# Optimization experiments

Hardware: AMD Instinct MI355X
Metric: run time of the kernel (lower is better)

The kernel has to match this reference:

```python
import jax, jax.numpy as jnp
import numpy as np

B, S, D_IN, H, D_HEAD = 4, 1024, 768, 12, 64


def setup_inputs() -> dict:
    key = jax.random.key(0)
    k1, k2, k3, k4 = jax.random.split(key, 4)
    x = jax.random.normal(k1, (B, S, D_IN), dtype=jnp.float32)
    # Per-head projection weights stored as [H, d_in, d_head] (equivalent to
    # nn.Linear weight [d_head, d_in] applied as x @ W.T), scaled like default init.
    scale = 1.0 / np.sqrt(D_IN)
    Wq = jax.random.normal(k2, (H, D_IN, D_HEAD), dtype=jnp.float32) * scale
    Wk = jax.random.normal(k3, (H, D_IN, D_HEAD), dtype=jnp.float32) * scale
    Wv = jax.random.normal(k4, (H, D_IN, D_HEAD), dtype=jnp.float32) * scale
    return {"x": x, "Wq": Wq, "Wk": Wk, "Wv": Wv}


def reference(x, Wq, Wk, Wv):
    # Vectorized over heads; faithful to per-head causal attention then concat.
    q = jnp.einsum("bsd,hde->bhse", x, Wq)  # [B,H,S,Dh]
    k = jnp.einsum("bsd,hde->bhse", x, Wk)
    v = jnp.einsum("bsd,hde->bhse", x, Wv)
    scale = 1.0 / jnp.sqrt(jnp.asarray(D_HEAD, dtype=q.dtype))
    scores = jnp.einsum("bhse,bhte->bhst", q, k) * scale  # [B,H,S,S]
    causal = jnp.tril(jnp.ones((S, S), dtype=bool))
    scores = jnp.where(causal, scores, jnp.finfo(scores.dtype).min)
    attn = jax.nn.softmax(scores, axis=-1)  # dropout p=0.0 (eval) -> identity
    ctx = jnp.einsum("bhst,bhte->bhse", attn, v)  # [B,H,S,Dh]
    # concat heads along last dim: [B,S,H*Dh]
    return jnp.transpose(ctx, (0, 2, 1, 3)).reshape(B, S, H * D_HEAD)
```

## Files before the change

kernel.cpp:

```cpp
#include <hip/hip_runtime.h>
#include <hip/hip_bf16.h>

#define NB 4
#define SS 1024
#define DIN 768
#define NH 12
#define DH 64

typedef float f32x4 __attribute__((ext_vector_type(4)));
typedef short bf16x8 __attribute__((ext_vector_type(8)));

static __device__ __forceinline__ unsigned short f2bf(float f) {
    __hip_bfloat16 h = __float2bfloat16(f);
    return *reinterpret_cast<unsigned short*>(&h);
}

static __device__ __forceinline__ float exp2_fast(float x) {
    return __builtin_amdgcn_exp2f(x);
}

static __device__ __forceinline__ void gload16(const void* g, void* l) {
    __builtin_amdgcn_global_load_lds(
        (const __attribute__((address_space(1))) void*)g,
        (__attribute__((address_space(3))) void*)l, 16, 0, 0);
}

__global__ void cast_x_kernel(const float* __restrict__ x, unsigned short* __restrict__ xb) {
    int i = (blockIdx.x * 256 + threadIdx.x) * 4;
    float4 v = *reinterpret_cast<const float4*>(x + i);
    ushort4 o;
    o.x = f2bf(v.x); o.y = f2bf(v.y); o.z = f2bf(v.z); o.w = f2bf(v.w);
    *reinterpret_cast<ushort4*>(xb + i) = o;
}

__global__ void transpose_w_kernel(const float* __restrict__ Wq, const float* __restrict__ Wk,
                                   const float* __restrict__ Wv, unsigned short* __restrict__ wt) {
    __shared__ float lds[64][68];
    int d0 = blockIdx.x * 64;
    int h  = blockIdx.y;
    int p  = blockIdx.z;
    const float* W = (p == 0) ? Wq : (p == 1) ? Wk : Wv;
    const float* base = W + (size_t)h * DIN * DH;
    int tid = threadIdx.x;
    int rr = tid >> 4, c4 = tid & 15;
#pragma unroll
    for (int i = 0; i < 4; ++i) {
        int d = i * 16 + rr;
        float4 v = *reinterpret_cast<const float4*>(base + (size_t)(d0 + d) * DH + c4 * 4);
        lds[d][c4 * 4 + 0] = v.x; lds[d][c4 * 4 + 1] = v.y;
        lds[d][c4 * 4 + 2] = v.z; lds[d][c4 * 4 + 3] = v.w;
    }
    __syncthreads();
    unsigned short* outp = wt + ((size_t)(p * NH + h) * DH) * DIN;
#pragma unroll
    for (int i = 0; i < 4; ++i) {
        int e = i * 16 + rr;
        int dc = c4 * 4;
        ushort4 o;
        o.x = f2bf(lds[dc + 0][e]); o.y = f2bf(lds[dc + 1][e]);
        o.z = f2bf(lds[dc + 2][e]); o.w = f2bf(lds[dc + 3][e]);
        *reinterpret_cast<ushort4*>(outp + (size_t)e * DIN + d0 + dc) = o;
    }
}

__global__ __launch_bounds__(256) void qkv_gemm_kernel(
    const unsigned short* __restrict__ xb, const unsigned short* __restrict__ wt,
    unsigned short* __restrict__ qb, unsigned short* __restrict__ kb,
    unsigned short* __restrict__ vT) {
    __shared__ __align__(16) unsigned char smem[28672];
    unsigned short* a_lds = (unsigned short*)smem;
    unsigned short* b_lds = (unsigned short*)(smem + 16384);

    int m0 = blockIdx.x * 128;
    int n0 = blockIdx.y * 96;
    int tid = threadIdx.x, lane = tid & 63, w = tid >> 6;
    int l15 = lane & 15, hi4 = (lane >> 4) * 4, hi8 = (lane >> 4) * 8;
    int wr = w >> 1, wc = w & 1;
    int srow = tid >> 3;
    int scolb = (tid & 7) * 16;
    int sw = (l15 & 7) << 4;

    f32x4 acc[4][3] = {};

    for (int k0 = 0; k0 < DIN; k0 += 64) {
        __syncthreads();
#pragma unroll
        for (int i = 0; i < 4; ++i) {
            int row = i * 32 + srow;
            int cb = scolb ^ ((row & 7) << 4);
            gload16(xb + (size_t)(m0 + row) * DIN + k0 + (cb >> 1), a_lds + row * 64 + (scolb >> 1));
        }
#pragma unroll
        for (int i = 0; i < 3; ++i) {
            int row = i * 32 + srow;
            int cb = scolb ^ ((row & 7) << 4);
            gload16(wt + (size_t)(n0 + row) * DIN + k0 + (cb >> 1), b_lds + row * 64 + (scolb >> 1));
        }
        __syncthreads();
#pragma unroll
        for (int kk = 0; kk < 64; kk += 32) {
            int cb = ((kk + hi8) * 2) ^ sw;
            bf16x8 af[4], bfr[3];
#pragma unroll
            for (int m = 0; m < 4; ++m)
                af[m] = *reinterpret_cast<const bf16x8*>(a_lds + (wr * 64 + m * 16 + l15) * 64 + (cb >> 1));
#pragma unroll
            for (int n = 0; n < 3; ++n)
                bfr[n] = *reinterpret_cast<const bf16x8*>(b_lds + (wc * 48 + n * 16 + l15) * 64 + (cb >> 1));
#pragma unroll
            for (int m = 0; m < 4; ++m)
#pragma unroll
                for (int n = 0; n < 3; ++n)
                    acc[m][n] = __builtin_amdgcn_mfma_f32_16x16x32_bf16(af[m], bfr[n], acc[m][n], 0, 0, 0);
        }
    }
    __syncthreads();

    int p  = n0 / 768;
    int cp = (n0 % 768) + wc * 48;
    int b  = m0 >> 10;
    int s_base = (m0 & 1023) + wr * 64;

    if (p < 2) {
        float qs = (p == 0) ? 0.180336880f : 1.0f;
        unsigned short* dstb = (p == 0) ? qb : kb;
#pragma unroll
        for (int m = 0; m < 4; ++m)
#pragma unroll
            for (int n = 0; n < 3; ++n)
#pragma unroll
                for (int r = 0; r < 4; ++r) {
                    int col = cp + n * 16 + l15;
                    int h = col >> 6, e = col & 63;
                    dstb[((size_t)(b * NH + h) * SS + s_base + m * 16 + hi4 + r) * DH + e] =
                        f2bf(acc[m][n][r] * qs);
                }
    } else {
        float* sc = (float*)smem + w * 784;
#pragma unroll
        for (int m = 0; m < 4; ++m) {
#pragma unroll
            for (int n = 0; n < 3; ++n)
#pragma unroll
                for (int r = 0; r < 4; ++r)
                    sc[(hi4 + r) * 49 + n * 16 + l15] = acc[m][n][r];
            if (lane < 48) {
                unsigned short vv[16];
#pragma unroll
                for (int t = 0; t < 16; ++t) vv[t] = f2bf(sc[t * 49 + lane]);
                int col = cp + lane;
                int h = col >> 6, e = col & 63;
                unsigned short* dst = vT + ((size_t)(b * NH + h) * DH + e) * SS + s_base + m * 16;
                *reinterpret_cast<uint4*>(dst)     = *reinterpret_cast<const uint4*>(vv);
                *reinterpret_cast<uint4*>(dst + 8) = *reinterpret_cast<const uint4*>(vv + 8);
            }
        }
    }
}

struct AttnCtx {
    const unsigned short* kg;
    const unsigned short* vg;
    unsigned short* k0lds; unsigned short* k1lds;
    unsigned short* v0lds; unsigned short* v1lds;
    unsigned short* pw;
    int srow, scolb, l15, hi4, hi8, sw;
};

static __device__ __forceinline__ void attn_stage(const AttnCtx& c, int buf, int kv) {
    unsigned short* kl = buf ? c.k1lds : c.k0lds;
    unsigned short* vl = buf ? c.v1lds : c.v0lds;
#pragma unroll
    for (int i = 0; i < 2; ++i) {
        int row = i * 32 + c.srow;
        int cb = c.scolb ^ ((row & 7) << 4);
        gload16(c.kg + (size_t)(kv * 64 + row) * DH + (cb >> 1), kl + row * 64 + (c.scolb >> 1));
        gload16(c.vg + (size_t)row * SS + kv * 64 + (cb >> 1),   vl + row * 64 + (c.scolb >> 1));
    }
}

template<bool DIAG>
static __device__ __forceinline__ void attn_step(
    const AttnCtx& c, int buf, int kv, int row_q,
    bf16x8 qf0, bf16x8 qf1, float m_r[4], float l_r[4], f32x4 o_acc[4]) {
    const unsigned short* kl = buf ? c.k1lds : c.k0lds;
    const unsigned short* vl = buf ? c.v1lds : c.v0lds;
    int l15 = c.l15, hi4 = c.hi4, hi8 = c.hi8, sw = c.sw;

    f32x4 sacc[4] = {};
#pragma unroll
    for (int s = 0; s < 2; ++s) {
        int cb = ((32 * s + hi8) * 2) ^ sw;
#pragma unroll
        for (int n = 0; n < 4; ++n) {
            bf16x8 kf = *reinterpret_cast<const bf16x8*>(kl + (16 * n + l15) * 64 + (cb >> 1));
            sacc[n] = __builtin_amdgcn_mfma_f32_16x16x32_bf16(s == 0 ? qf0 : qf1, kf, sacc[n], 0, 0, 0);
        }
    }
    float pv[4][4];
#pragma unroll
    for (int n = 0; n < 4; ++n)
#pragma unroll
        for (int r = 0; r < 4; ++r) {
            float sv = sacc[n][r];
            if (DIAG && (kv * 64 + 16 * n + l15) > (row_q + hi4 + r)) sv = -INFINITY;
            pv[n][r] = sv;
        }
#pragma unroll
    for (int r = 0; r < 4; ++r) {
        float mx = fmaxf(fmaxf(pv[0][r], pv[1][r]), fmaxf(pv[2][r], pv[3][r]));
        mx = fmaxf(mx, __shfl_xor(mx, 1));
        mx = fmaxf(mx, __shfl_xor(mx, 2));
        mx = fmaxf(mx, __shfl_xor(mx, 4));
        mx = fmaxf(mx, __shfl_xor(mx, 8));
        float m_new = fmaxf(m_r[r], mx);
        float s0 = exp2_fast(pv[0][r] - m_new);
        float s1 = exp2_fast(pv[1][r] - m_new);
        float s2 = exp2_fast(pv[2][r] - m_new);
        float s3 = exp2_fast(pv[3][r] - m_new);
        pv[0][r] = s0; pv[1][r] = s1; pv[2][r] = s2; pv[3][r] = s3;
        float sum = (s0 + s1) + (s2 + s3);
        sum += __shfl_xor(sum, 1);
        sum += __shfl_xor(sum, 2);
        sum += __shfl_xor(sum, 4);
        sum += __shfl_xor(sum, 8);
        float alpha = exp2_fast(m_r[r] - m_new);
        l_r[r] = l_r[r] * alpha + sum;
        m_r[r] = m_new;
#pragma unroll
        for (int n = 0; n < 4; ++n) o_acc[n][r] *= alpha;
    }
#pragma unroll
    for (int n = 0; n < 4; ++n)
#pragma unroll
        for (int r = 0; r < 4; ++r)
            c.pw[(hi4 + r) * 72 + 16 * n + l15] = f2bf(pv[n][r]);
    bf16x8 pa0 = *reinterpret_cast<const bf16x8*>(c.pw + l15 * 72 + hi8);
    bf16x8 pa1 = *reinterpret_cast<const bf16x8*>(c.pw + l15 * 72 + 32 + hi8);
#pragma unroll
    for (int s = 0; s < 2; ++s) {
        int cb = ((32 * s + hi8) * 2) ^ sw;
#pragma unroll
        for (int n = 0; n < 4; ++n) {
            bf16x8 vf = *reinterpret_cast<const bf16x8*>(vl + (16 * n + l15) * 64 + (cb >> 1));
            o_acc[n] = __builtin_amdgcn_mfma_f32_16x16x32_bf16(s == 0 ? pa0 : pa1, vf, o_acc[n], 0, 0, 0);
        }
    }
}

__global__ __launch_bounds__(256) void attn_kernel(
    const unsigned short* __restrict__ qb, const unsigned short* __restrict__ kb,
    const unsigned short* __restrict__ vT, float* __restrict__ out) {
    __shared__ __align__(16) unsigned short k_lds[2][64 * 64];
    __shared__ __align__(16) unsigned short v_lds[2][64 * 64];
    __shared__ __align__(16) unsigned short p_lds[4 * 16 * 72];

    int bid = blockIdx.x;
    int qi = 15 - bid / 48;
    int rem = bid % 48;
    int h = rem % 12, b = rem / 12;
    int q0 = qi * 64;
    int tid = threadIdx.x, lane = tid & 63, w = tid >> 6;
    int l15 = lane & 15, hi4 = (lane >> 4) * 4, hi8 = (lane >> 4) * 8;
    size_t bh = (size_t)(b * NH + h);

    AttnCtx c;
    c.kg = kb + bh * SS * DH;
    c.vg = vT + bh * DH * SS;
    c.k0lds = k_lds[0]; c.k1lds = k_lds[1];
    c.v0lds = v_lds[0]; c.v1lds = v_lds[1];
    c.pw = p_lds + w * 16 * 72;
    c.srow = tid >> 3; c.scolb = (tid & 7) * 16;
    c.l15 = l15; c.hi4 = hi4; c.hi8 = hi8; c.sw = (l15 & 7) << 4;

    const unsigned short* qp = qb + (bh * SS + q0 + 16 * w + l15) * DH;
    bf16x8 qf0 = *reinterpret_cast<const bf16x8*>(qp + hi8);
    bf16x8 qf1 = *reinterpret_cast<const bf16x8*>(qp + 32 + hi8);

    float m_r[4] = {-INFINITY, -INFINITY, -INFINITY, -INFINITY};
    float l_r[4] = {0.f, 0.f, 0.f, 0.f};
    f32x4 o_acc[4] = {};
    int row_q = q0 + 16 * w;

    attn_stage(c, 0, 0);
    __syncthreads();
    for (int kv = 0; kv < qi; ++kv) {
        int cur = kv & 1;
        attn_stage(c, cur ^ 1, kv + 1);
        attn_step<false>(c, cur, kv, row_q, qf0, qf1, m_r, l_r, o_acc);
        __syncthreads();
    }
    attn_step<true>(c, qi & 1, qi, row_q, qf0, qf1, m_r, l_r, o_acc);

    float inv[4];
#pragma unroll
    for (int r = 0; r < 4; ++r) inv[r] = 1.f / l_r[r];
#pragma unroll
    for (int n = 0; n < 4; ++n)
#pragma unroll
        for (int r = 0; r < 4; ++r) {
            int q = q0 + 16 * w + hi4 + r;
            int e = 16 * n + l15;
            out[((size_t)b * SS + q) * (NH * DH) + h * DH + e] = o_acc[n][r] * inv[r];
        }
}

extern "C" void kernel_launch(void* const* d_in, const int* in_sizes, int n_in,
                              void* d_out, int out_size, void* d_ws, size_t ws_size,
                              hipStream_t stream) {
    const float* x  = (const float*)d_in[0];
    const float* Wq = (const float*)d_in[1];
    const float* Wk = (const float*)d_in[2];
    const float* Wv = (const float*)d_in[3];
    float* out = (float*)d_out;

    char* ws = (char*)d_ws;
    unsigned short* xb = (unsigned short*)ws;
    unsigned short* wt = (unsigned short*)(ws +  6291456);
    unsigned short* qb = (unsigned short*)(ws +  9830400);
    unsigned short* kb = (unsigned short*)(ws + 16121856);
    unsigned short* vT = (unsigned short*)(ws + 22413312);

    hipLaunchKernelGGL(cast_x_kernel,      dim3(3072),      dim3(256), 0, stream, x, xb);
    hipLaunchKernelGGL(transpose_w_kernel, dim3(12, 12, 3), dim3(256), 0, stream, Wq, Wk, Wv, wt);
    hipLaunchKernelGGL(qkv_gemm_kernel,    dim3(32, 24),    dim3(256), 0, stream, xb, wt, qb, kb, vT);
    hipLaunchKernelGGL(attn_kernel,        dim3(768),       dim3(256), 0, stream, qb, kb, vT, out);
}
```

Measured before the change: 124.8 us.

## Transpose attention MFMA operands, lazy softmax rescale, vectorized output store

Swaps the MFMA operand order so each lane owns one query row. The softmax max and sum reductions now need only two cross-lane shuffles, and each lane holds a single m/l scalar instead of four. The running-max rescale is skipped unless some row's max grows by more than 8 (log2 units), which cuts exp and multiply work but lets the unnormalized values grow up to 2^8. It also adds s_setprio around the MFMA blocks and packs P writes as 32-bit words. The output goes through an LDS transpose so it can be written with 16-byte vector stores.

```diff
diff --git a/kernel.cpp b/kernel.cpp
--- a/kernel.cpp
+++ b/kernel.cpp
@@ -161,15 +161,14 @@
 struct AttnCtx {
     const unsigned short* kg;
     const unsigned short* vg;
-    unsigned short* k0lds; unsigned short* k1lds;
-    unsigned short* v0lds; unsigned short* v1lds;
+    char* smem;
     unsigned short* pw;
-    int srow, scolb, l15, hi4, hi8, sw;
+    int srow, scolb, l15, hi, sw;
 };
 
 static __device__ __forceinline__ void attn_stage(const AttnCtx& c, int buf, int kv) {
-    unsigned short* kl = buf ? c.k1lds : c.k0lds;
-    unsigned short* vl = buf ? c.v1lds : c.v0lds;
+    unsigned short* kl = (unsigned short*)(c.smem + buf * 8192);
+    unsigned short* vl = (unsigned short*)(c.smem + 16384 + buf * 8192);
 #pragma unroll
     for (int i = 0; i < 2; ++i) {
         int row = i * 32 + c.srow;
@@ -181,79 +180,95 @@
 
 template<bool DIAG>
 static __device__ __forceinline__ void attn_step(
-    const AttnCtx& c, int buf, int kv, int row_q,
-    bf16x8 qf0, bf16x8 qf1, float m_r[4], float l_r[4], f32x4 o_acc[4]) {
-    const unsigned short* kl = buf ? c.k1lds : c.k0lds;
-    const unsigned short* vl = buf ? c.v1lds : c.v0lds;
-    int l15 = c.l15, hi4 = c.hi4, hi8 = c.hi8, sw = c.sw;
+    const AttnCtx& c, int buf, int kv, int qg,
+    bf16x8 qf0, bf16x8 qf1, float& m_r, float& l_r, f32x4 o_acc[4]) {
+    const unsigned short* kl = (const unsigned short*)(c.smem + buf * 8192);
+    const unsigned short* vl = (const unsigned short*)(c.smem + 16384 + buf * 8192);
+    int l15 = c.l15, hi = c.hi, sw = c.sw;
+    int hi4 = hi * 4, hi8 = hi * 8;
 
     f32x4 sacc[4] = {};
+    __builtin_amdgcn_s_setprio(1);
 #pragma unroll
     for (int s = 0; s < 2; ++s) {
         int cb = ((32 * s + hi8) * 2) ^ sw;
 #pragma unroll
         for (int n = 0; n < 4; ++n) {
             bf16x8 kf = *reinterpret_cast<const bf16x8*>(kl + (16 * n + l15) * 64 + (cb >> 1));
-            sacc[n] = __builtin_amdgcn_mfma_f32_16x16x32_bf16(s == 0 ? qf0 : qf1, kf, sacc[n], 0, 0, 0);
-        }
-    }
+            sacc[n] = __builtin_amdgcn_mfma_f32_16x16x32_bf16(kf, s == 0 ? qf0 : qf1, sacc[n], 0, 0, 0);
+        }
+    }
+    __builtin_amdgcn_s_setprio(0);
+
     float pv[4][4];
 #pragma unroll
     for (int n = 0; n < 4; ++n)
 #pragma unroll
         for (int r = 0; r < 4; ++r) {
             float sv = sacc[n][r];
-            if (DIAG && (kv * 64 + 16 * n + l15) > (row_q + hi4 + r)) sv = -INFINITY;
+            if (DIAG && (kv * 64 + 16 * n + hi4 + r) > qg) sv = -INFINITY;
             pv[n][r] = sv;
         }
-#pragma unroll
-    for (int r = 0; r < 4; ++r) {
-        float mx = fmaxf(fmaxf(pv[0][r], pv[1][r]), fmaxf(pv[2][r], pv[3][r]));
-        mx = fmaxf(mx, __shfl_xor(mx, 1));
-        mx = fmaxf(mx, __shfl_xor(mx, 2));
-        mx = fmaxf(mx, __shfl_xor(mx, 4));
-        mx = fmaxf(mx, __shfl_xor(mx, 8));
-        float m_new = fmaxf(m_r[r], mx);
-        float s0 = exp2_fast(pv[0][r] - m_new);
-        float s1 = exp2_fast(pv[1][r] - m_new);
-        float s2 = exp2_fast(pv[2][r] - m_new);
-        float s3 = exp2_fast(pv[3][r] - m_new);
-        pv[0][r] = s0; pv[1][r] = s1; pv[2][r] = s2; pv[3][r] = s3;
-        float sum = (s0 + s1) + (s2 + s3);
-        sum += __shfl_xor(sum, 1);
-        sum += __shfl_xor(sum, 2);
-        sum += __shfl_xor(sum, 4);
-        sum += __shfl_xor(sum, 8);
-        float alpha = exp2_fast(m_r[r] - m_new);
-        l_r[r] = l_r[r] * alpha + sum;
-        m_r[r] = m_new;
-#pragma unroll
-        for (int n = 0; n < 4; ++n) o_acc[n][r] *= alpha;
-    }
+
+    float mn[4];
 #pragma unroll
     for (int n = 0; n < 4; ++n)
-#pragma unroll
-        for (int r = 0; r < 4; ++r)
-            c.pw[(hi4 + r) * 72 + 16 * n + l15] = f2bf(pv[n][r]);
+        mn[n] = fmaxf(fmaxf(pv[n][0], pv[n][1]), fmaxf(pv[n][2], pv[n][3]));
+    float mx = fmaxf(fmaxf(mn[0], mn[1]), fmaxf(mn[2], mn[3]));
+    mx = fmaxf(mx, __shfl_xor(mx, 16));
+    mx = fmaxf(mx, __shfl_xor(mx, 32));
+
+    if (!__all(mx - m_r <= 8.0f)) {
+        float m_new = fmaxf(m_r, mx);
+        float alpha = exp2_fast(m_r - m_new);
+        l_r *= alpha;
+#pragma unroll
+        for (int n = 0; n < 4; ++n)
+#pragma unroll
+            for (int r = 0; r < 4; ++r) o_acc[n][r] *= alpha;
+        m_r = m_new;
+    }
+    float sn[4];
+#pragma unroll
+    for (int n = 0; n < 4; ++n) {
+#pragma unroll
+        for (int r = 0; r < 4; ++r) pv[n][r] = exp2_fast(pv[n][r] - m_r);
+        sn[n] = (pv[n][0] + pv[n][1]) + (pv[n][2] + pv[n][3]);
+    }
+    float sum = (sn[0] + sn[1]) + (sn[2] + sn[3]);
+    sum += __shfl_xor(sum, 16);
+    sum += __shfl_xor(sum, 32);
+    l_r += sum;
+
+    unsigned int* pwu = (unsigned int*)c.pw;
+#pragma unroll
+    for (int n = 0; n < 4; ++n)
+#pragma unroll
+        for (int p2 = 0; p2 < 2; ++p2) {
+            unsigned int w32 = (unsigned int)f2bf(pv[n][2 * p2]) |
+                               ((unsigned int)f2bf(pv[n][2 * p2 + 1]) << 16);
+            pwu[l15 * 36 + 8 * n + 2 * hi + p2] = w32;
+        }
     bf16x8 pa0 = *reinterpret_cast<const bf16x8*>(c.pw + l15 * 72 + hi8);
     bf16x8 pa1 = *reinterpret_cast<const bf16x8*>(c.pw + l15 * 72 + 32 + hi8);
+
+    __builtin_amdgcn_s_setprio(1);
 #pragma unroll
     for (int s = 0; s < 2; ++s) {
         int cb = ((32 * s + hi8) * 2) ^ sw;
 #pragma unroll
         for (int n = 0; n < 4; ++n) {
             bf16x8 vf = *reinterpret_cast<const bf16x8*>(vl + (16 * n + l15) * 64 + (cb >> 1));
-            o_acc[n] = __builtin_amdgcn_mfma_f32_16x16x32_bf16(s == 0 ? pa0 : pa1, vf, o_acc[n], 0, 0, 0);
-        }
-    }
+            o_acc[n] = __builtin_amdgcn_mfma_f32_16x16x32_bf16(vf, s == 0 ? pa0 : pa1, o_acc[n], 0, 0, 0);
+        }
+    }
+    __builtin_amdgcn_s_setprio(0);
 }
 
 __global__ __launch_bounds__(256) void attn_kernel(
     const unsigned short* __restrict__ qb, const unsigned short* __restrict__ kb,
     const unsigned short* __restrict__ vT, float* __restrict__ out) {
-    __shared__ __align__(16) unsigned short k_lds[2][64 * 64];
-    __shared__ __align__(16) unsigned short v_lds[2][64 * 64];
-    __shared__ __align__(16) unsigned short p_lds[4 * 16 * 72];
+    __shared__ __align__(16) char smem[41984];
 
     int bid = blockIdx.x;
     int qi = 15 - bid / 48;
@@ -261,48 +276,49 @@
     int h = rem % 12, b = rem / 12;
     int q0 = qi * 64;
     int tid = threadIdx.x, lane = tid & 63, w = tid >> 6;
-    int l15 = lane & 15, hi4 = (lane >> 4) * 4, hi8 = (lane >> 4) * 8;
+    int l15 = lane & 15, hi = lane >> 4;
     size_t bh = (size_t)(b * NH + h);
 
     AttnCtx c;
     c.kg = kb + bh * SS * DH;
     c.vg = vT + bh * DH * SS;
-    c.k0lds = k_lds[0]; c.k1lds = k_lds[1];
-    c.v0lds = v_lds[0]; c.v1lds = v_lds[1];
-    c.pw = p_lds + w * 16 * 72;
+    c.smem = smem;
+    c.pw = (unsigned short*)(smem + 32768) + w * 1152;
     c.srow = tid >> 3; c.scolb = (tid & 7) * 16;
-    c.l15 = l15; c.hi4 = hi4; c.hi8 = hi8; c.sw = (l15 & 7) << 4;
-
-    const unsigned short* qp = qb + (bh * SS + q0 + 16 * w + l15) * DH;
-    bf16x8 qf0 = *reinterpret_cast<const bf16x8*>(qp + hi8);
-    bf16x8 qf1 = *reinterpret_cast<const bf16x8*>(qp + 32 + hi8);
-
-    float m_r[4] = {-INFINITY, -INFINITY, -INFINITY, -INFINITY};
-    float l_r[4] = {0.f, 0.f, 0.f, 0.f};
+    c.l15 = l15; c.hi = hi; c.sw = (l15 & 7) << 4;
+
+    int qg = q0 + 16 * w + l15;
+    const unsigned short* qp = qb + (bh * SS + qg) * DH;
+    bf16x8 qf0 = *reinterpret_cast<const bf16x8*>(qp + hi * 8);
+    bf16x8 qf1 = *reinterpret_cast<const bf16x8*>(qp + 32 + hi * 8);
+
+    float m_r = -INFINITY, l_r = 0.f;
     f32x4 o_acc[4] = {};
-    int row_q = q0 + 16 * w;
 
     attn_stage(c, 0, 0);
     __syncthreads();
     for (int kv = 0; kv < qi; ++kv) {
-        int cur = kv & 1;
-        attn_stage(c, cur ^ 1, kv + 1);
-        attn_step<false>(c, cur, kv, row_q, qf0, qf1, m_r, l_r, o_acc);
+        attn_stage(c, (kv & 1) ^ 1, kv + 1);
+        attn_step<false>(c, kv & 1, kv, qg, qf0, qf1, m_r, l_r, o_acc);
         __syncthreads();
     }
-    attn_step<true>(c, qi & 1, qi, row_q, qf0, qf1, m_r, l_r, o_acc);
-
-    float inv[4];
-#pragma unroll
-    for (int r = 0; r < 4; ++r) inv[r] = 1.f / l_r[r];
+    attn_step<true>(c, qi & 1, qi, qg, qf0, qf1, m_r, l_r, o_acc);
+    __syncthreads();
+
+    float inv = 1.f / l_r;
+    float* sc = (float*)(smem + w * 4352);
 #pragma unroll
     for (int n = 0; n < 4; ++n)
 #pragma unroll
-        for (int r = 0; r < 4; ++r) {
-            int q = q0 + 16 * w + hi4 + r;
-            int e = 16 * n + l15;
-            out[((size_t)b * SS + q) * (NH * DH) + h * DH + e] = o_acc[n][r] * inv[r];
-        }
+        for (int r = 0; r < 4; ++r)
+            sc[l15 * 68 + 16 * n + hi * 4 + r] = o_acc[n][r] * inv;
+    __builtin_amdgcn_s_waitcnt(0);
+#pragma unroll
+    for (int j = 0; j < 4; ++j) {
+        f32x4 v = *reinterpret_cast<const f32x4*>(sc + l15 * 68 + j * 16 + hi * 4);
+        *reinterpret_cast<f32x4*>(out + ((size_t)b * SS + q0 + 16 * w + l15) * (NH * DH)
+                                  + h * DH + j * 16 + hi * 4) = v;
+    }
 }
 
 extern "C" void kernel_launch(void* const* d_in, const int* in_sizes, int n_in,
```

Result: faster. 118.8 us (-4.8%).
